# Kernel optimization log

Hardware: AMD Instinct MI355X
Metric: run time of the kernel (lower is better)

Reference implementation:

```python
import jax, jax.numpy as jnp
import numpy as np

N = 100000   # nodes
E = 1600000  # edges
NC = 10000   # candidates
G = 1000     # graphs
ND = 32      # node_emb_dim
ED = 8       # edge_emb_dim
L = 4        # num_layers


def setup_inputs() -> dict:
    key = jax.random.key(0)
    ks = jax.random.split(key, 12)
    s = 0.1
    return {
        "x": jax.random.normal(ks[0], (N, 2), dtype=jnp.float32),
        "edge_attr": jax.random.normal(ks[1], (E, 1), dtype=jnp.float32),
        "Wn_in": jax.random.normal(ks[2], (2, ND)) * s,
        "bn_in": jnp.zeros((ND,)),
        "We_in": jax.random.normal(ks[3], (1, ED)) * s,
        "be_in": jnp.zeros((ED,)),
        "We_l": jax.random.normal(ks[4], (L, 2 * ND + ED, ED)) * s,
        "be_l": jnp.zeros((L, ED)),
        "Wn_l": jax.random.normal(ks[5], (L, ND + ED, ND)) * s,
        "bn_l": jnp.zeros((L, ND)),
        "Wout": jax.random.normal(ks[6], (ND, 1)) * s,
        "bout": jnp.zeros((1,)),
        "edge_index": jax.random.randint(ks[7], (2, E), 0, N),
        "batch": jnp.sort(jax.random.randint(ks[8], (N,), 0, G)),
        "candidate_idxs": jax.random.randint(ks[9], (NC,), 0, N),
    }


def reference(x, edge_attr, Wn_in, bn_in, We_in, be_in, We_l, be_l, Wn_l, bn_l,
              Wout, bout, edge_index, batch, candidate_idxs):
    h = x @ Wn_in + bn_in            # [N, ND]
    e = edge_attr @ We_in + be_in    # [E, ED]
    src, dst = edge_index[0], edge_index[1]
    for l in range(L):
        # edge update: MLP on [x_src, x_dst, edge_attr]
        m = jnp.concatenate([h[src], h[dst], e], axis=-1)        # [E, 2*ND+ED]
        new_e = jax.nn.relu(m @ We_l[l] + be_l[l])               # [E, ED]
        # aggregate (aggr='add') messages at destination nodes
        agg = jax.ops.segment_sum(new_e, dst, num_segments=N)    # [N, ED]
        new_h = jax.nn.relu(jnp.concatenate([h, agg], axis=-1) @ Wn_l[l] + bn_l[l])
        h = h + new_h   # residual
        e = e + new_e   # residual
    logits = (h[candidate_idxs] @ Wout + bout)[:, 0]             # [NC]
    seg = batch[candidate_idxs]                                  # [NC] graph ids
    # scatter_log_softmax over per-graph candidate groups
    mx = jax.ops.segment_max(logits, seg, num_segments=G)
    shifted = logits - mx[seg]
    lse = jnp.log(jax.ops.segment_sum(jnp.exp(shifted), seg, num_segments=G))
    return shifted - lse[seg]
```

## Files before the change

kernel.cpp:

```cpp
#include <hip/hip_runtime.h>

#define ND 32
#define ED 8
#define NL 4
#define NG 1000
#define NBC_MAX 512
#define CHUNK 8192
#define CHUNK_H 4096

typedef unsigned short u16;

__device__ __forceinline__ int xcd_swizzle(int b, int nb) {
  int per = nb >> 3;
  return (b < (per << 3)) ? ((b & 7) * per + (b >> 3)) : b;
}


__device__ __forceinline__ unsigned pack2(float a, float b) {
  unsigned r;
  asm("v_cvt_pk_bf16_f32 %0, %1, %2" : "=v"(r) : "v"(a), "v"(b));
  return r;
}
__device__ __forceinline__ float bf_round(float f) {
  unsigned r;
  asm("v_cvt_pk_bf16_f32 %0, %1, %2" : "=v"(r) : "v"(f), "v"(f));
  return __uint_as_float(r << 16);
}
__device__ __forceinline__ void cvt8(uint4 p, float* o) {
  o[0] = __uint_as_float(p.x << 16); o[1] = __uint_as_float(p.x & 0xffff0000u);
  o[2] = __uint_as_float(p.y << 16); o[3] = __uint_as_float(p.y & 0xffff0000u);
  o[4] = __uint_as_float(p.z << 16); o[5] = __uint_as_float(p.z & 0xffff0000u);
  o[6] = __uint_as_float(p.w << 16); o[7] = __uint_as_float(p.w & 0xffff0000u);
}
__device__ __forceinline__ uint4 pack8(const float* v) {
  uint4 o;
  o.x = pack2(v[0], v[1]); o.y = pack2(v[2], v[3]);
  o.z = pack2(v[4], v[5]); o.w = pack2(v[6], v[7]);
  return o;
}


__global__ void k_chist(const int* __restrict__ dst, int* __restrict__ bcnt,
                        int E, int nbc) {
  __shared__ int lcnt[NBC_MAX];
  for (int b = threadIdx.x; b < nbc; b += blockDim.x) lcnt[b] = 0;
  __syncthreads();
  int e0 = blockIdx.x * CHUNK_H;
  int e1 = min(e0 + CHUNK_H, E);
  for (int i = e0 + threadIdx.x; i < e1; i += blockDim.x)
    atomicAdd(&lcnt[dst[i] >> 8], 1);
  __syncthreads();
  for (int b = threadIdx.x; b < nbc; b += blockDim.x)
    if (lcnt[b]) atomicAdd(&bcnt[b], lcnt[b]);
}

__global__ void k_cscan(const int* __restrict__ bcnt, int* __restrict__ bbase,
                        int nbc) {
  __shared__ int s[NBC_MAX];
  int tid = threadIdx.x;
  if (nbc <= NBC_MAX) {
    int v = (tid < nbc) ? bcnt[tid] : 0;
    s[tid] = v;
    __syncthreads();
    for (int st = 1; st < NBC_MAX; st <<= 1) {
      int t = (tid >= st) ? s[tid - st] : 0;
      __syncthreads();
      s[tid] += t;
      __syncthreads();
    }
    if (tid < nbc) bbase[tid] = s[tid] - v;
    if (tid == nbc - 1) bbase[nbc] = s[tid];
  } else if (tid == 0) {
    int run = 0;
    for (int i = 0; i < nbc; ++i) { bbase[i] = run; run += bcnt[i]; }
    bbase[nbc] = run;
  }
}

__global__ void k_binA(const int* __restrict__ src, const int* __restrict__ dst,
                       const float* __restrict__ ea,
                       const int* __restrict__ bbase, int* __restrict__ cursor_c,
                       uint2* __restrict__ binned, int E, int nbc) {
  __shared__ int lcnt[NBC_MAX];
  __shared__ int lbase[NBC_MAX];
  for (int b = threadIdx.x; b < nbc; b += blockDim.x) lcnt[b] = 0;
  __syncthreads();
  int e0 = blockIdx.x * CHUNK;
  int e1 = min(e0 + CHUNK, E);
  for (int i = e0 + threadIdx.x; i < e1; i += blockDim.x)
    atomicAdd(&lcnt[dst[i] >> 8], 1);
  __syncthreads();
  for (int b = threadIdx.x; b < nbc; b += blockDim.x) {
    int c = lcnt[b];
    lbase[b] = c ? (bbase[b] + atomicAdd(&cursor_c[b], c)) : 0;
  }
  __syncthreads();
  for (int i = e0 + threadIdx.x; i < e1; i += blockDim.x) {
    int d = dst[i];
    int pos = atomicAdd(&lbase[d >> 8], 1);
    binned[pos] = make_uint2((unsigned)src[i] | ((unsigned)(d & 255) << 24),
                             __float_as_uint(ea[i]));
  }
}

__global__ void k_binB_init(const uint2* __restrict__ binned,
                            const int* __restrict__ bbase,
                            int* __restrict__ ssrc, float* __restrict__ ea_s,
                            int* __restrict__ noffs,
                            const float* __restrict__ x,
                            const float* __restrict__ Wni,
                            const float* __restrict__ bni,
                            const float* __restrict__ We0,
                            const float* __restrict__ be0,
                            u16* __restrict__ h,
                            u16* __restrict__ zs, u16* __restrict__ zd,
                            int N) {
  __shared__ int hist[256];
  __shared__ int scn[256];
  int b = blockIdx.x;
  int base = bbase[b], end = bbase[b + 1];
  int node0 = b << 8;
  int nn = min(256, N - node0);
  hist[threadIdx.x] = 0;
  __syncthreads();
  for (int p = base + threadIdx.x; p < end; p += blockDim.x)
    atomicAdd(&hist[binned[p].x >> 24], 1);
  __syncthreads();
  int v = hist[threadIdx.x];
  scn[threadIdx.x] = v;
  __syncthreads();
  for (int st = 1; st < 256; st <<= 1) {
    int t = (threadIdx.x >= (unsigned)st) ? scn[threadIdx.x - st] : 0;
    __syncthreads();
    scn[threadIdx.x] += t;
    __syncthreads();
  }
  int excl = base + scn[threadIdx.x] - v;
  if ((int)threadIdx.x < nn) noffs[node0 + threadIdx.x] = excl;
  if (threadIdx.x == 0) noffs[min(node0 + 256, N)] = end;
  hist[threadIdx.x] = excl;
  __syncthreads();
  for (int p = base + threadIdx.x; p < end; p += blockDim.x) {
    uint2 rec = binned[p];
    int dl = (int)(rec.x >> 24);
    int pos = atomicAdd(&hist[dl], 1);
    ssrc[pos] = (int)(rec.x & 0xffffffu);
    ea_s[pos] = __uint_as_float(rec.y);
  }
  int n = node0 + threadIdx.x;
  if (n < N) {
    float x0 = x[2 * n], x1 = x[2 * n + 1];
    float vv[ND];
#pragma unroll
    for (int d = 0; d < ND; ++d)
      vv[d] = bf_round(fmaf(x0, Wni[d], fmaf(x1, Wni[ND + d], bni[d])));
    uint4* h4 = reinterpret_cast<uint4*>(h + (size_t)n * ND);
#pragma unroll
    for (int q = 0; q < 4; ++q) h4[q] = pack8(&vv[q * 8]);
    float zsv[ED], zdv[ED];
#pragma unroll
    for (int j = 0; j < ED; ++j) { zsv[j] = 0.0f; zdv[j] = be0[j]; }
#pragma unroll
    for (int k = 0; k < ND; ++k)
#pragma unroll
      for (int j = 0; j < ED; ++j) {
        zsv[j] = fmaf(vv[k], We0[k * ED + j], zsv[j]);
        zdv[j] = fmaf(vv[k], We0[(ND + k) * ED + j], zdv[j]);
      }
    *reinterpret_cast<uint4*>(zs + (size_t)n * ED) = pack8(zsv);
    *reinterpret_cast<uint4*>(zd + (size_t)n * ED) = pack8(zdv);
  }
}

template <int L0>
__global__ void k_layer(u16* __restrict__ h,
                        u16* __restrict__ e,
                        const float* __restrict__ ea_s,
                        const int* __restrict__ ssrc,
                        const int* __restrict__ noffs,
                        const u16* __restrict__ zs,
                        const u16* __restrict__ zd,
                        const float* __restrict__ Wei,
                        const float* __restrict__ bei,
                        const float* __restrict__ W3,
                        const float* __restrict__ Wn,
                        const float* __restrict__ bn,
                        const float* __restrict__ Wen,
                        const float* __restrict__ ben,
                        u16* __restrict__ zs_n, u16* __restrict__ zd_n,
                        int N) {
  int t = xcd_swizzle(blockIdx.x, gridDim.x) * blockDim.x + threadIdx.x;
  int n = t >> 3;
  int g = t & 7;
  if (n >= N) return;
  int o0 = noffs[n], o1 = noffs[n + 1];
  float zdv[ED];
  cvt8(*reinterpret_cast<const uint4*>(zd + (size_t)n * ED), zdv);
  const uint4* zs4 = reinterpret_cast<const uint4*>(zs);
  const uint4* e4c = reinterpret_cast<const uint4*>(e);
  uint4* e4 = reinterpret_cast<uint4*>(e);
  float av[ED];
#pragma unroll
  for (int j = 0; j < ED; ++j) av[j] = 0.0f;

  int p = o0 + g;
  int sA = 0, sB = 0;
  uint4 eA = make_uint4(0, 0, 0, 0), eB = make_uint4(0, 0, 0, 0);
  float aA = 0.0f, aB = 0.0f;
  uint4 zA = make_uint4(0, 0, 0, 0);
  if (p < o1) {
    sA = ssrc[p];
    if (L0) aA = ea_s[p]; else eA = e4c[p];
    zA = zs4[sA];
  }
  if (p + 8 < o1) {
    sB = ssrc[p + 8];
    if (L0) aB = ea_s[p + 8]; else eB = e4c[p + 8];
  }
  for (; p < o1; ) {
    int pn = p + 8, pc = p + 16;
    uint4 zB = make_uint4(0, 0, 0, 0);
    if (pn < o1) zB = zs4[sB];
    int sC = 0; uint4 eC = make_uint4(0, 0, 0, 0); float aC = 0.0f;
    if (pc < o1) {
      sC = ssrc[pc];
      if (L0) aC = ea_s[pc]; else eC = e4c[pc];
    }
    float zsv[ED], ein[ED], acc[ED];
    cvt8(zA, zsv);
    if (L0) {
#pragma unroll
      for (int j = 0; j < ED; ++j) ein[j] = fmaf(aA, Wei[j], bei[j]);
    } else {
      cvt8(eA, ein);
    }
#pragma unroll
    for (int j = 0; j < ED; ++j) acc[j] = zsv[j] + zdv[j];
#pragma unroll
    for (int k = 0; k < ED; ++k)
#pragma unroll
      for (int j = 0; j < ED; ++j)
        acc[j] = fmaf(ein[k], W3[k * ED + j], acc[j]);
    float eo[ED];
#pragma unroll
    for (int j = 0; j < ED; ++j) {
      float r = fmaxf(acc[j], 0.0f);
      av[j] += r;
      eo[j] = ein[j] + r;
    }
    e4[p] = pack8(eo);
    p = pn;
    sA = sB; eA = eB; aA = aB; zA = zB;
    sB = sC; eB = eC; aB = aC;
  }
#pragma unroll
  for (int j = 0; j < ED; ++j) {
    av[j] += __shfl_xor(av[j], 1);
    av[j] += __shfl_xor(av[j], 2);
    av[j] += __shfl_xor(av[j], 4);
  }
  uint4* h4 = reinterpret_cast<uint4*>(h + (size_t)n * ND);
  float hv[ND];
#pragma unroll
  for (int q = 0; q < 4; ++q) cvt8(h4[q], &hv[q * 8]);
  const int j0 = g * 4;
  float acc4[4];
#pragma unroll
  for (int jj = 0; jj < 4; ++jj) acc4[jj] = bn[j0 + jj];
#pragma unroll
  for (int k = 0; k < ND; ++k)
#pragma unroll
    for (int jj = 0; jj < 4; ++jj)
      acc4[jj] = fmaf(hv[k], Wn[k * ND + j0 + jj], acc4[jj]);
#pragma unroll
  for (int k = 0; k < ED; ++k)
#pragma unroll
    for (int jj = 0; jj < 4; ++jj)
      acc4[jj] = fmaf(av[k], Wn[(ND + k) * ND + j0 + jj], acc4[jj]);
  float hn4[4];
#pragma unroll
  for (int jj = 0; jj < 4; ++jj)
    hn4[jj] = bf_round(hv[j0 + jj] + fmaxf(acc4[jj], 0.0f));
  reinterpret_cast<uint2*>(h + (size_t)n * ND)[g] =
      make_uint2(pack2(hn4[0], hn4[1]), pack2(hn4[2], hn4[3]));
  float pz[2 * ED];
#pragma unroll
  for (int j = 0; j < 2 * ED; ++j) pz[j] = 0.0f;
#pragma unroll
  for (int kk = 0; kk < 4; ++kk) {
    float hk = hn4[kk];
    int krow = j0 + kk;
#pragma unroll
    for (int j = 0; j < ED; ++j) {
      pz[j] = fmaf(hk, Wen[krow * ED + j], pz[j]);
      pz[ED + j] = fmaf(hk, Wen[(ND + krow) * ED + j], pz[ED + j]);
    }
  }
#pragma unroll
  for (int j = 0; j < 2 * ED; ++j) {
    pz[j] += __shfl_xor(pz[j], 1);
    pz[j] += __shfl_xor(pz[j], 2);
    pz[j] += __shfl_xor(pz[j], 4);
  }
  if (g == 0) {
    *reinterpret_cast<uint4*>(zs_n + (size_t)n * ED) = pack8(pz);
  } else if (g == 1) {
    float zdo[ED];
#pragma unroll
    for (int j = 0; j < ED; ++j) zdo[j] = pz[ED + j] + ben[j];
    *reinterpret_cast<uint4*>(zd_n + (size_t)n * ED) = pack8(zdo);
  }
}


__device__ __forceinline__ unsigned int enc_f32(float f) {
  unsigned int bits = __float_as_uint(f);
  return (bits & 0x80000000u) ? ~bits : (bits | 0x80000000u);
}
__device__ __forceinline__ float dec_f32(unsigned int u) {
  unsigned int bits = (u & 0x80000000u) ? (u ^ 0x80000000u) : ~u;
  return __uint_as_float(bits);
}

__global__ void k_cand(const u16* __restrict__ h,
                       const u16* __restrict__ e,
                       const u16* __restrict__ zs,
                       const u16* __restrict__ zd,
                       const int* __restrict__ ssrc,
                       const int* __restrict__ noffs,
                       const int* __restrict__ cand,
                       const int* __restrict__ batch,
                       const float* __restrict__ W3,
                       const float* __restrict__ Wn,
                       const float* __restrict__ bn,
                       const float* __restrict__ Wout,
                       const float* __restrict__ bout,
                       float* __restrict__ logits,
                       int* __restrict__ seg,
                       unsigned int* __restrict__ mxu,
                       int NC) {
  int t = blockIdx.x * blockDim.x + threadIdx.x;
  int c = t >> 4, g = t & 15;
  if (c >= NC) return;
  int n = cand[c];
  int o0 = noffs[n], o1 = noffs[n + 1];
  const uint4* h4 = reinterpret_cast<const uint4*>(h + (size_t)n * ND);
  uint4 hq0 = h4[0], hq1 = h4[1], hq2 = h4[2], hq3 = h4[3];
  float zdv[ED];
  cvt8(*reinterpret_cast<const uint4*>(zd + (size_t)n * ED), zdv);
  const uint4* zs4 = reinterpret_cast<const uint4*>(zs);
  const uint4* e4c = reinterpret_cast<const uint4*>(e);
  float av[ED];
#pragma unroll
  for (int j = 0; j < ED; ++j) av[j] = 0.0f;

  auto cand_one = [&](uint4 z_, uint4 e_) {
    float zsv[ED], ein[ED], acc[ED];
    cvt8(z_, zsv);
    cvt8(e_, ein);
#pragma unroll
    for (int j = 0; j < ED; ++j) acc[j] = zsv[j] + zdv[j];
#pragma unroll
    for (int k = 0; k < ED; ++k)
#pragma unroll
      for (int j = 0; j < ED; ++j)
        acc[j] = fmaf(ein[k], W3[k * ED + j], acc[j]);
#pragma unroll
    for (int j = 0; j < ED; ++j) av[j] += fmaxf(acc[j], 0.0f);
  };

  for (int base = o0 + g; base < o1; base += 32) {
    bool v1 = base + 16 < o1;
    int pa = base;
    int pb = v1 ? base + 16 : base;
    int sa = ssrc[pa], sb = ssrc[pb];
    uint4 Ea = e4c[pa], Eb = e4c[pb];
    uint4 Za = zs4[sa], Zb = zs4[sb];
    cand_one(Za, Ea);
    if (v1) cand_one(Zb, Eb);
  }
#pragma unroll
  for (int j = 0; j < ED; ++j) {
    av[j] += __shfl_xor(av[j], 1);
    av[j] += __shfl_xor(av[j], 2);
    av[j] += __shfl_xor(av[j], 4);
    av[j] += __shfl_xor(av[j], 8);
  }
  float hv[ND];
  cvt8(hq0, &hv[0]); cvt8(hq1, &hv[8]); cvt8(hq2, &hv[16]); cvt8(hq3, &hv[24]);
  const int j0 = g * 2;
  float acc2[2];
#pragma unroll
  for (int jj = 0; jj < 2; ++jj) acc2[jj] = bn[j0 + jj];
#pragma unroll
  for (int k = 0; k < ND; ++k)
#pragma unroll
    for (int jj = 0; jj < 2; ++jj)
      acc2[jj] = fmaf(hv[k], Wn[k * ND + j0 + jj], acc2[jj]);
#pragma unroll
  for (int k = 0; k < ED; ++k)
#pragma unroll
    for (int jj = 0; jj < 2; ++jj)
      acc2[jj] = fmaf(av[k], Wn[(ND + k) * ND + j0 + jj], acc2[jj]);
  float lg = 0.0f;
#pragma unroll
  for (int jj = 0; jj < 2; ++jj)
    lg = fmaf(hv[j0 + jj] + fmaxf(acc2[jj], 0.0f), Wout[j0 + jj], lg);
  lg += __shfl_xor(lg, 1);
  lg += __shfl_xor(lg, 2);
  lg += __shfl_xor(lg, 4);
  lg += __shfl_xor(lg, 8);
  if (g == 0) {
    lg += bout[0];
    logits[c] = lg;
    int gr = batch[n];
    seg[c] = gr;
    atomicMax(&mxu[gr], enc_f32(lg));
  }
}

__global__ void k_expsum(float* __restrict__ logits,
                         const int* __restrict__ seg,
                         const unsigned int* __restrict__ mxu,
                         float* __restrict__ sum,
                         int NC) {
  int c = blockIdx.x * blockDim.x + threadIdx.x;
  if (c >= NC) return;
  int g = seg[c];
  float sh = logits[c] - dec_f32(mxu[g]);
  logits[c] = sh;
  atomicAdd(&sum[g], expf(sh));
}

__global__ void k_final(const float* __restrict__ shifted,
                        const int* __restrict__ seg,
                        const float* __restrict__ sum,
                        float* __restrict__ out, int NC) {
  int c = blockIdx.x * blockDim.x + threadIdx.x;
  if (c >= NC) return;
  out[c] = shifted[c] - logf(sum[seg[c]]);
}


extern "C" void kernel_launch(void* const* d_in, const int* in_sizes, int n_in,
                              void* d_out, int out_size, void* d_ws, size_t ws_size,
                              hipStream_t stream) {
  const float* x       = (const float*)d_in[0];
  const float* ea      = (const float*)d_in[1];
  const float* Wn_in   = (const float*)d_in[2];
  const float* bn_in   = (const float*)d_in[3];
  const float* We_in   = (const float*)d_in[4];
  const float* be_in   = (const float*)d_in[5];
  const float* We_l    = (const float*)d_in[6];
  const float* be_l    = (const float*)d_in[7];
  const float* Wn_l    = (const float*)d_in[8];
  const float* bn_l    = (const float*)d_in[9];
  const float* Wout    = (const float*)d_in[10];
  const float* bout    = (const float*)d_in[11];
  const int* edge_index= (const int*)d_in[12];
  const int* batch     = (const int*)d_in[13];
  const int* cand      = (const int*)d_in[14];

  const int N  = in_sizes[13];
  const int E  = in_sizes[1];
  const int NC = in_sizes[14];
  const int nbc = (N + 255) >> 8;

  char* ws = (char*)d_ws;
  uint2* binned = (uint2*)ws; ws += (size_t)E * sizeof(uint2);
  int*   ssrc   = (int*)ws;   ws += (size_t)E * sizeof(int);
  float* ea_s   = (float*)ws; ws += (size_t)E * sizeof(float);
  u16*   h      = (u16*)ws;   ws += (size_t)N * ND * sizeof(u16);
  u16*   e      = (u16*)ws;   ws += (size_t)E * ED * sizeof(u16);
  u16*   zs0    = (u16*)ws;   ws += (size_t)N * ED * sizeof(u16);
  u16*   zd0    = (u16*)ws;   ws += (size_t)N * ED * sizeof(u16);
  u16*   zs1    = (u16*)ws;   ws += (size_t)N * ED * sizeof(u16);
  u16*   zd1    = (u16*)ws;   ws += (size_t)N * ED * sizeof(u16);
  int*   noffs  = (int*)ws;   ws += ((size_t)N + 4) * sizeof(int);
  int*   bcnt   = (int*)ws;   ws += (size_t)NBC_MAX * sizeof(int);
  int*   cursor = (int*)ws;   ws += (size_t)NBC_MAX * sizeof(int);
  unsigned int* mxu = (unsigned int*)ws; ws += (size_t)NG * sizeof(unsigned int);
  float* sum    = (float*)ws; ws += (size_t)NG * sizeof(float);
  int*   bbase  = (int*)ws;   ws += ((size_t)NBC_MAX + 4) * sizeof(int);
  float* logits = (float*)ws; ws += (size_t)NC * sizeof(float);
  int*   seg    = (int*)ws;   ws += (size_t)NC * sizeof(int);

  const int* srcp = edge_index;
  const int* dstp = edge_index + E;
  const int blk = 256;
  const size_t WE_STRIDE = (size_t)(2 * ND + ED) * ED;

  hipMemsetAsync(bcnt, 0, (2 * (size_t)NBC_MAX + 2 * (size_t)NG) * sizeof(int),
                 stream);

  k_chist<<<(E + CHUNK_H - 1) / CHUNK_H, 1024, 0, stream>>>(dstp, bcnt, E, nbc);
  k_cscan<<<1, NBC_MAX, 0, stream>>>(bcnt, bbase, nbc);
  k_binA<<<(E + CHUNK - 1) / CHUNK, 1024, 0, stream>>>(srcp, dstp, ea, bbase,
                                                       cursor, binned, E, nbc);
  k_binB_init<<<nbc, 256, 0, stream>>>(binned, bbase, ssrc, ea_s, noffs,
                                       x, Wn_in, bn_in, We_l, be_l,
                                       h, zs0, zd0, N);

  const int ngrid8 = (N + 31) / 32;
  u16* zsc = zs0; u16* zdc = zd0;
  u16* zsn = zs1; u16* zdn = zd1;
  for (int l = 0; l < NL - 1; ++l) {
    const float* W3 = We_l + l * WE_STRIDE + (size_t)2 * ND * ED;
    const float* Wn = Wn_l + (size_t)l * (ND + ED) * ND;
    const float* bn = bn_l + (size_t)l * ND;
    const float* Wen = We_l + (l + 1) * WE_STRIDE;
    const float* ben = be_l + (size_t)(l + 1) * ED;
    if (l == 0) {
      k_layer<1><<<ngrid8, 256, 0, stream>>>(
          h, e, ea_s, ssrc, noffs, zsc, zdc, We_in, be_in, W3, Wn, bn,
          Wen, ben, zsn, zdn, N);
    } else {
      k_layer<0><<<ngrid8, 256, 0, stream>>>(
          h, e, ea_s, ssrc, noffs, zsc, zdc, We_in, be_in, W3, Wn, bn,
          Wen, ben, zsn, zdn, N);
    }
    u16* t;
    t = zsc; zsc = zsn; zsn = t;
    t = zdc; zdc = zdn; zdn = t;
  }

  {
    const int l = NL - 1;
    const float* W3 = We_l + l * WE_STRIDE + (size_t)2 * ND * ED;
    const float* Wn = Wn_l + (size_t)l * (ND + ED) * ND;
    const float* bn = bn_l + (size_t)l * ND;
    k_cand<<<((size_t)NC * 16 + 255) / 256, 256, 0, stream>>>(
        h, e, zsc, zdc, ssrc, noffs, cand, batch, W3, Wn, bn, Wout, bout,
        logits, seg, mxu, NC);
  }
  k_expsum<<<(NC + blk - 1) / blk, blk, 0, stream>>>(logits, seg, mxu, sum, NC);
  k_final<<<(NC + blk - 1) / blk, blk, 0, stream>>>(logits, seg, sum,
                                                    (float*)d_out, NC);
}
```

Measured before the change: 331.8 us.

## Replace two-level bucket sort with direct per-node counting sort using global atomics

Builds the destination-sorted CSR by counting edges per node with global atomics, scanning node counts in one block, and scattering edges via per-node atomic cursors, fused with node embedding init. This removes the intermediate binned buffer and the two-pass coarse/fine bucketing. In exchange it relies on heavy global atomic traffic, a serial-heavy single-block scan, and edge order within a node becomes nondeterministic.

```diff
diff --git a/kernel.cpp b/kernel.cpp
--- a/kernel.cpp
+++ b/kernel.cpp
@@ -4,9 +4,6 @@
 #define ED 8
 #define NL 4
 #define NG 1000
-#define NBC_MAX 512
-#define CHUNK 8192
-#define CHUNK_H 4096
 
 typedef unsigned short u16;
 
@@ -40,121 +37,68 @@
 }
 
 
-__global__ void k_chist(const int* __restrict__ dst, int* __restrict__ bcnt,
-                        int E, int nbc) {
-  __shared__ int lcnt[NBC_MAX];
-  for (int b = threadIdx.x; b < nbc; b += blockDim.x) lcnt[b] = 0;
+__global__ void k_nhist(const int* __restrict__ dst, int* __restrict__ ncnt,
+                        int E) {
+  int i = blockIdx.x * blockDim.x + threadIdx.x;
+  if (i < E) atomicAdd(&ncnt[dst[i]], 1);
+}
+
+__global__ void k_nscan(const int* __restrict__ ncnt, int* __restrict__ noffs,
+                        int* __restrict__ cur, int N, int E) {
+  __shared__ int s[1024];
+  int t = threadIdx.x;
+  int C = (N + 1023) >> 10;
+  int lo = t * C, hi = min(lo + C, N);
+  int run = 0;
+  for (int i = lo; i < hi; ++i) {
+    int v = ncnt[i];
+    noffs[i] = run;
+    run += v;
+  }
+  s[t] = run;
   __syncthreads();
-  int e0 = blockIdx.x * CHUNK_H;
-  int e1 = min(e0 + CHUNK_H, E);
-  for (int i = e0 + threadIdx.x; i < e1; i += blockDim.x)
-    atomicAdd(&lcnt[dst[i] >> 8], 1);
-  __syncthreads();
-  for (int b = threadIdx.x; b < nbc; b += blockDim.x)
-    if (lcnt[b]) atomicAdd(&bcnt[b], lcnt[b]);
-}
-
-__global__ void k_cscan(const int* __restrict__ bcnt, int* __restrict__ bbase,
-                        int nbc) {
-  __shared__ int s[NBC_MAX];
-  int tid = threadIdx.x;
-  if (nbc <= NBC_MAX) {
-    int v = (tid < nbc) ? bcnt[tid] : 0;
-    s[tid] = v;
+  for (int st = 1; st < 1024; st <<= 1) {
+    int v = (t >= st) ? s[t - st] : 0;
     __syncthreads();
-    for (int st = 1; st < NBC_MAX; st <<= 1) {
-      int t = (tid >= st) ? s[tid - st] : 0;
-      __syncthreads();
-      s[tid] += t;
-      __syncthreads();
-    }
-    if (tid < nbc) bbase[tid] = s[tid] - v;
-    if (tid == nbc - 1) bbase[nbc] = s[tid];
-  } else if (tid == 0) {
-    int run = 0;
-    for (int i = 0; i < nbc; ++i) { bbase[i] = run; run += bcnt[i]; }
-    bbase[nbc] = run;
-  }
-}
-
-__global__ void k_binA(const int* __restrict__ src, const int* __restrict__ dst,
-                       const float* __restrict__ ea,
-                       const int* __restrict__ bbase, int* __restrict__ cursor_c,
-                       uint2* __restrict__ binned, int E, int nbc) {
-  __shared__ int lcnt[NBC_MAX];
-  __shared__ int lbase[NBC_MAX];
-  for (int b = threadIdx.x; b < nbc; b += blockDim.x) lcnt[b] = 0;
-  __syncthreads();
-  int e0 = blockIdx.x * CHUNK;
-  int e1 = min(e0 + CHUNK, E);
-  for (int i = e0 + threadIdx.x; i < e1; i += blockDim.x)
-    atomicAdd(&lcnt[dst[i] >> 8], 1);
-  __syncthreads();
-  for (int b = threadIdx.x; b < nbc; b += blockDim.x) {
-    int c = lcnt[b];
-    lbase[b] = c ? (bbase[b] + atomicAdd(&cursor_c[b], c)) : 0;
-  }
-  __syncthreads();
-  for (int i = e0 + threadIdx.x; i < e1; i += blockDim.x) {
+    s[t] += v;
+    __syncthreads();
+  }
+  int base = s[t] - run;
+  for (int i = lo; i < hi; ++i) {
+    int v = noffs[i] + base;
+    noffs[i] = v;
+    cur[i] = v;
+  }
+  if (t == 0) noffs[N] = E;
+}
+
+__global__ void k_scatter_init(const int* __restrict__ src,
+                               const int* __restrict__ dst,
+                               const float* __restrict__ ea,
+                               int* __restrict__ cur,
+                               int* __restrict__ ssrc, float* __restrict__ ea_s,
+                               const float* __restrict__ x,
+                               const float* __restrict__ Wni,
+                               const float* __restrict__ bni,
+                               const float* __restrict__ We0,
+                               const float* __restrict__ be0,
+                               u16* __restrict__ h,
+                               u16* __restrict__ zs, u16* __restrict__ zd,
+                               int E, int N) {
+  int i = blockIdx.x * blockDim.x + threadIdx.x;
+  if (i < E) {
     int d = dst[i];
-    int pos = atomicAdd(&lbase[d >> 8], 1);
-    binned[pos] = make_uint2((unsigned)src[i] | ((unsigned)(d & 255) << 24),
-                             __float_as_uint(ea[i]));
-  }
-}
-
-__global__ void k_binB_init(const uint2* __restrict__ binned,
-                            const int* __restrict__ bbase,
-                            int* __restrict__ ssrc, float* __restrict__ ea_s,
-                            int* __restrict__ noffs,
-                            const float* __restrict__ x,
-                            const float* __restrict__ Wni,
-                            const float* __restrict__ bni,
-                            const float* __restrict__ We0,
-                            const float* __restrict__ be0,
-                            u16* __restrict__ h,
-                            u16* __restrict__ zs, u16* __restrict__ zd,
-                            int N) {
-  __shared__ int hist[256];
-  __shared__ int scn[256];
-  int b = blockIdx.x;
-  int base = bbase[b], end = bbase[b + 1];
-  int node0 = b << 8;
-  int nn = min(256, N - node0);
-  hist[threadIdx.x] = 0;
-  __syncthreads();
-  for (int p = base + threadIdx.x; p < end; p += blockDim.x)
-    atomicAdd(&hist[binned[p].x >> 24], 1);
-  __syncthreads();
-  int v = hist[threadIdx.x];
-  scn[threadIdx.x] = v;
-  __syncthreads();
-  for (int st = 1; st < 256; st <<= 1) {
-    int t = (threadIdx.x >= (unsigned)st) ? scn[threadIdx.x - st] : 0;
-    __syncthreads();
-    scn[threadIdx.x] += t;
-    __syncthreads();
-  }
-  int excl = base + scn[threadIdx.x] - v;
-  if ((int)threadIdx.x < nn) noffs[node0 + threadIdx.x] = excl;
-  if (threadIdx.x == 0) noffs[min(node0 + 256, N)] = end;
-  hist[threadIdx.x] = excl;
-  __syncthreads();
-  for (int p = base + threadIdx.x; p < end; p += blockDim.x) {
-    uint2 rec = binned[p];
-    int dl = (int)(rec.x >> 24);
-    int pos = atomicAdd(&hist[dl], 1);
-    ssrc[pos] = (int)(rec.x & 0xffffffu);
-    ea_s[pos] = __uint_as_float(rec.y);
-  }
-  int n = node0 + threadIdx.x;
-  if (n < N) {
-    float x0 = x[2 * n], x1 = x[2 * n + 1];
+    int pos = atomicAdd(&cur[d], 1);
+    ssrc[pos] = src[i];
+    ea_s[pos] = ea[i];
+  }
+  if (i < N) {
+    float x0 = x[2 * i], x1 = x[2 * i + 1];
     float vv[ND];
 #pragma unroll
     for (int d = 0; d < ND; ++d)
       vv[d] = bf_round(fmaf(x0, Wni[d], fmaf(x1, Wni[ND + d], bni[d])));
-    uint4* h4 = reinterpret_cast<uint4*>(h + (size_t)n * ND);
+    uint4* h4 = reinterpret_cast<uint4*>(h + (size_t)i * ND);
 #pragma unroll
     for (int q = 0; q < 4; ++q) h4[q] = pack8(&vv[q * 8]);
     float zsv[ED], zdv[ED];
@@ -167,8 +111,8 @@
         zsv[j] = fmaf(vv[k], We0[k * ED + j], zsv[j]);
         zdv[j] = fmaf(vv[k], We0[(ND + k) * ED + j], zdv[j]);
       }
-    *reinterpret_cast<uint4*>(zs + (size_t)n * ED) = pack8(zsv);
-    *reinterpret_cast<uint4*>(zd + (size_t)n * ED) = pack8(zdv);
+    *reinterpret_cast<uint4*>(zs + (size_t)i * ED) = pack8(zsv);
+    *reinterpret_cast<uint4*>(zd + (size_t)i * ED) = pack8(zdv);
   }
 }
 
@@ -464,10 +408,8 @@
   const int N  = in_sizes[13];
   const int E  = in_sizes[1];
   const int NC = in_sizes[14];
-  const int nbc = (N + 255) >> 8;
 
   char* ws = (char*)d_ws;
-  uint2* binned = (uint2*)ws; ws += (size_t)E * sizeof(uint2);
   int*   ssrc   = (int*)ws;   ws += (size_t)E * sizeof(int);
   float* ea_s   = (float*)ws; ws += (size_t)E * sizeof(float);
   u16*   h      = (u16*)ws;   ws += (size_t)N * ND * sizeof(u16);
@@ -477,11 +419,10 @@
   u16*   zs1    = (u16*)ws;   ws += (size_t)N * ED * sizeof(u16);
   u16*   zd1    = (u16*)ws;   ws += (size_t)N * ED * sizeof(u16);
   int*   noffs  = (int*)ws;   ws += ((size_t)N + 4) * sizeof(int);
-  int*   bcnt   = (int*)ws;   ws += (size_t)NBC_MAX * sizeof(int);
-  int*   cursor = (int*)ws;   ws += (size_t)NBC_MAX * sizeof(int);
+  int*   cur    = (int*)ws;   ws += ((size_t)N + 4) * sizeof(int);
+  int*   ncnt   = (int*)ws;   ws += (size_t)N * sizeof(int);
   unsigned int* mxu = (unsigned int*)ws; ws += (size_t)NG * sizeof(unsigned int);
   float* sum    = (float*)ws; ws += (size_t)NG * sizeof(float);
-  int*   bbase  = (int*)ws;   ws += ((size_t)NBC_MAX + 4) * sizeof(int);
   float* logits = (float*)ws; ws += (size_t)NC * sizeof(float);
   int*   seg    = (int*)ws;   ws += (size_t)NC * sizeof(int);
 
@@ -490,16 +431,13 @@
   const int blk = 256;
   const size_t WE_STRIDE = (size_t)(2 * ND + ED) * ED;
 
-  hipMemsetAsync(bcnt, 0, (2 * (size_t)NBC_MAX + 2 * (size_t)NG) * sizeof(int),
-                 stream);
-
-  k_chist<<<(E + CHUNK_H - 1) / CHUNK_H, 1024, 0, stream>>>(dstp, bcnt, E, nbc);
-  k_cscan<<<1, NBC_MAX, 0, stream>>>(bcnt, bbase, nbc);
-  k_binA<<<(E + CHUNK - 1) / CHUNK, 1024, 0, stream>>>(srcp, dstp, ea, bbase,
-                                                       cursor, binned, E, nbc);
-  k_binB_init<<<nbc, 256, 0, stream>>>(binned, bbase, ssrc, ea_s, noffs,
-                                       x, Wn_in, bn_in, We_l, be_l,
-                                       h, zs0, zd0, N);
+  hipMemsetAsync(ncnt, 0, ((size_t)N + 2 * (size_t)NG) * sizeof(int), stream);
+
+  k_nhist<<<(E + blk - 1) / blk, blk, 0, stream>>>(dstp, ncnt, E);
+  k_nscan<<<1, 1024, 0, stream>>>(ncnt, noffs, cur, N, E);
+  k_scatter_init<<<(E + blk - 1) / blk, blk, 0, stream>>>(
+      srcp, dstp, ea, cur, ssrc, ea_s, x, Wn_in, bn_in, We_l, be_l,
+      h, zs0, zd0, E, N);
 
   const int ngrid8 = (N + 31) / 32;
   u16* zsc = zs0; u16* zdc = zd0;
```

After: 734.8 us. 121% more time.

## Fuse layer, candidate and softmax kernels into one cooperative persistent kernel

Applied to the files above, without the earlier changes.

Replaces the per-layer k_layer launches plus k_cand, k_expsum and k_final with a single cooperative kernel that loops over layers using grid-stride loops and grid.sync() between stages. The goal is to remove several kernel launch gaps and tail effects between short dependent stages. In exchange the grid is capped at occupancy-limited resident blocks. The mega kernel uses the union of both bodies' registers, which may lower occupancy and slow the memory-bound layer phases. A fallback to the old multi-kernel path is kept if the cooperative launch fails.

```diff
diff --git a/kernel.cpp b/kernel.cpp
--- a/kernel.cpp
+++ b/kernel.cpp
@@ -1,4 +1,7 @@
 #include <hip/hip_runtime.h>
+#include <hip/hip_cooperative_groups.h>
+
+namespace cg = cooperative_groups;
 
 #define ND 32
 #define ED 8
@@ -7,6 +10,7 @@
 #define NBC_MAX 512
 #define CHUNK 8192
 #define CHUNK_H 4096
+#define WE_STRIDE ((size_t)(2 * ND + ED) * ED)
 
 typedef unsigned short u16;
 
@@ -37,6 +41,15 @@
   o.x = pack2(v[0], v[1]); o.y = pack2(v[2], v[3]);
   o.z = pack2(v[4], v[5]); o.w = pack2(v[6], v[7]);
   return o;
+}
+
+__device__ __forceinline__ unsigned int enc_f32(float f) {
+  unsigned int bits = __float_as_uint(f);
+  return (bits & 0x80000000u) ? ~bits : (bits | 0x80000000u);
+}
+__device__ __forceinline__ float dec_f32(unsigned int u) {
+  unsigned int bits = (u & 0x80000000u) ? (u ^ 0x80000000u) : ~u;
+  return __uint_as_float(bits);
 }
 
 
@@ -173,26 +186,15 @@
 }
 
 template <int L0>
-__global__ void k_layer(u16* __restrict__ h,
-                        u16* __restrict__ e,
-                        const float* __restrict__ ea_s,
-                        const int* __restrict__ ssrc,
-                        const int* __restrict__ noffs,
-                        const u16* __restrict__ zs,
-                        const u16* __restrict__ zd,
-                        const float* __restrict__ Wei,
-                        const float* __restrict__ bei,
-                        const float* __restrict__ W3,
-                        const float* __restrict__ Wn,
-                        const float* __restrict__ bn,
-                        const float* __restrict__ Wen,
-                        const float* __restrict__ ben,
-                        u16* __restrict__ zs_n, u16* __restrict__ zd_n,
-                        int N) {
-  int t = xcd_swizzle(blockIdx.x, gridDim.x) * blockDim.x + threadIdx.x;
-  int n = t >> 3;
-  int g = t & 7;
-  if (n >= N) return;
+__device__ __forceinline__ void layer_body(
+    int n, int g, u16* __restrict__ h, u16* __restrict__ e,
+    const float* __restrict__ ea_s, const int* __restrict__ ssrc,
+    const int* __restrict__ noffs, const u16* __restrict__ zs,
+    const u16* __restrict__ zd, const float* __restrict__ Wei,
+    const float* __restrict__ bei, const float* __restrict__ W3,
+    const float* __restrict__ Wn, const float* __restrict__ bn,
+    const float* __restrict__ Wen, const float* __restrict__ ben,
+    u16* __restrict__ zs_n, u16* __restrict__ zd_n) {
   int o0 = noffs[n], o1 = noffs[n + 1];
   float zdv[ED];
   cvt8(*reinterpret_cast<const uint4*>(zd + (size_t)n * ED), zdv);
@@ -312,36 +314,15 @@
   }
 }
 
-
-__device__ __forceinline__ unsigned int enc_f32(float f) {
-  unsigned int bits = __float_as_uint(f);
-  return (bits & 0x80000000u) ? ~bits : (bits | 0x80000000u);
-}
-__device__ __forceinline__ float dec_f32(unsigned int u) {
-  unsigned int bits = (u & 0x80000000u) ? (u ^ 0x80000000u) : ~u;
-  return __uint_as_float(bits);
-}
-
-__global__ void k_cand(const u16* __restrict__ h,
-                       const u16* __restrict__ e,
-                       const u16* __restrict__ zs,
-                       const u16* __restrict__ zd,
-                       const int* __restrict__ ssrc,
-                       const int* __restrict__ noffs,
-                       const int* __restrict__ cand,
-                       const int* __restrict__ batch,
-                       const float* __restrict__ W3,
-                       const float* __restrict__ Wn,
-                       const float* __restrict__ bn,
-                       const float* __restrict__ Wout,
-                       const float* __restrict__ bout,
-                       float* __restrict__ logits,
-                       int* __restrict__ seg,
-                       unsigned int* __restrict__ mxu,
-                       int NC) {
-  int t = blockIdx.x * blockDim.x + threadIdx.x;
-  int c = t >> 4, g = t & 15;
-  if (c >= NC) return;
+__device__ __forceinline__ void cand_body(
+    int c, int g, const u16* __restrict__ h, const u16* __restrict__ e,
+    const u16* __restrict__ zs, const u16* __restrict__ zd,
+    const int* __restrict__ ssrc, const int* __restrict__ noffs,
+    const int* __restrict__ cand, const int* __restrict__ batch,
+    const float* __restrict__ W3, const float* __restrict__ Wn,
+    const float* __restrict__ bn, const float* __restrict__ Wout,
+    const float* __restrict__ bout, float* __restrict__ logits,
+    int* __restrict__ seg, unsigned int* __restrict__ mxu) {
   int n = cand[c];
   int o0 = noffs[n], o1 = noffs[n + 1];
   const uint4* h4 = reinterpret_cast<const uint4*>(h + (size_t)n * ND);
@@ -419,11 +400,53 @@
   }
 }
 
+
+template <int L0>
+__global__ void k_layer(u16* __restrict__ h, u16* __restrict__ e,
+                        const float* __restrict__ ea_s,
+                        const int* __restrict__ ssrc,
+                        const int* __restrict__ noffs,
+                        const u16* __restrict__ zs, const u16* __restrict__ zd,
+                        const float* __restrict__ Wei,
+                        const float* __restrict__ bei,
+                        const float* __restrict__ W3,
+                        const float* __restrict__ Wn,
+                        const float* __restrict__ bn,
+                        const float* __restrict__ Wen,
+                        const float* __restrict__ ben,
+                        u16* __restrict__ zs_n, u16* __restrict__ zd_n,
+                        int N) {
+  int t = xcd_swizzle(blockIdx.x, gridDim.x) * blockDim.x + threadIdx.x;
+  int n = t >> 3, g = t & 7;
+  if (n >= N) return;
+  layer_body<L0>(n, g, h, e, ea_s, ssrc, noffs, zs, zd, Wei, bei, W3, Wn, bn,
+                 Wen, ben, zs_n, zd_n);
+}
+
+__global__ void k_cand(const u16* __restrict__ h, const u16* __restrict__ e,
+                       const u16* __restrict__ zs, const u16* __restrict__ zd,
+                       const int* __restrict__ ssrc,
+                       const int* __restrict__ noffs,
+                       const int* __restrict__ cand,
+                       const int* __restrict__ batch,
+                       const float* __restrict__ W3,
+                       const float* __restrict__ Wn,
+                       const float* __restrict__ bn,
+                       const float* __restrict__ Wout,
+                       const float* __restrict__ bout,
+                       float* __restrict__ logits, int* __restrict__ seg,
+                       unsigned int* __restrict__ mxu, int NC) {
+  int t = blockIdx.x * blockDim.x + threadIdx.x;
+  int c = t >> 4, g = t & 15;
+  if (c >= NC) return;
+  cand_body(c, g, h, e, zs, zd, ssrc, noffs, cand, batch, W3, Wn, bn, Wout,
+            bout, logits, seg, mxu);
+}
+
 __global__ void k_expsum(float* __restrict__ logits,
                          const int* __restrict__ seg,
                          const unsigned int* __restrict__ mxu,
-                         float* __restrict__ sum,
-                         int NC) {
+                         float* __restrict__ sum, int NC) {
   int c = blockIdx.x * blockDim.x + threadIdx.x;
   if (c >= NC) return;
   int g = seg[c];
@@ -439,6 +462,74 @@
   int c = blockIdx.x * blockDim.x + threadIdx.x;
   if (c >= NC) return;
   out[c] = shifted[c] - logf(sum[seg[c]]);
+}
+
+
+struct MegaArgs {
+  u16 *h, *e;
+  const float* ea_s;
+  const int* ssrc;
+  const int* noffs;
+  u16 *zs0, *zd0, *zs1, *zd1;
+  const float *We_in, *be_in, *We_l, *be_l, *Wn_l, *bn_l;
+  const int *cand, *batch;
+  const float *Wout, *bout;
+  float* logits;
+  int* seg;
+  unsigned int* mxu;
+  float* sum;
+  float* out;
+  int N, NC;
+};
+
+__global__ void k_mega(MegaArgs a) {
+  cg::grid_group grid = cg::this_grid();
+  const long gid = (long)blockIdx.x * blockDim.x + threadIdx.x;
+  const long GT = (long)gridDim.x * blockDim.x;
+  u16 *zsc = a.zs0, *zdc = a.zd0, *zsn = a.zs1, *zdn = a.zd1;
+  for (int l = 0; l < NL - 1; ++l) {
+    const float* W3 = a.We_l + l * WE_STRIDE + (size_t)2 * ND * ED;
+    const float* Wn = a.Wn_l + (size_t)l * (ND + ED) * ND;
+    const float* bn = a.bn_l + (size_t)l * ND;
+    const float* Wen = a.We_l + (l + 1) * WE_STRIDE;
+    const float* ben = a.be_l + (size_t)(l + 1) * ED;
+    const long TT = (long)a.N * 8;
+    for (long t = gid; t < TT; t += GT) {
+      int n = (int)(t >> 3), g = (int)(t & 7);
+      if (l == 0)
+        layer_body<1>(n, g, a.h, a.e, a.ea_s, a.ssrc, a.noffs, zsc, zdc,
+                      a.We_in, a.be_in, W3, Wn, bn, Wen, ben, zsn, zdn);
+      else
+        layer_body<0>(n, g, a.h, a.e, a.ea_s, a.ssrc, a.noffs, zsc, zdc,
+                      a.We_in, a.be_in, W3, Wn, bn, Wen, ben, zsn, zdn);
+    }
+    grid.sync();
+    u16* tp;
+    tp = zsc; zsc = zsn; zsn = tp;
+    tp = zdc; zdc = zdn; zdn = tp;
+  }
+  {
+    const int l = NL - 1;
+    const float* W3 = a.We_l + l * WE_STRIDE + (size_t)2 * ND * ED;
+    const float* Wn = a.Wn_l + (size_t)l * (ND + ED) * ND;
+    const float* bn = a.bn_l + (size_t)l * ND;
+    const long TT = (long)a.NC * 16;
+    for (long t = gid; t < TT; t += GT) {
+      int c = (int)(t >> 4), g = (int)(t & 15);
+      cand_body(c, g, a.h, a.e, zsc, zdc, a.ssrc, a.noffs, a.cand, a.batch,
+                W3, Wn, bn, a.Wout, a.bout, a.logits, a.seg, a.mxu);
+    }
+  }
+  grid.sync();
+  for (long c = gid; c < a.NC; c += GT) {
+    int g = a.seg[c];
+    float sh = a.logits[c] - dec_f32(a.mxu[g]);
+    a.logits[c] = sh;
+    atomicAdd(&a.sum[g], expf(sh));
+  }
+  grid.sync();
+  for (long c = gid; c < a.NC; c += GT)
+    a.out[c] = a.logits[c] - logf(a.sum[a.seg[c]]);
 }
 
 
@@ -488,7 +579,6 @@
   const int* srcp = edge_index;
   const int* dstp = edge_index + E;
   const int blk = 256;
-  const size_t WE_STRIDE = (size_t)(2 * ND + ED) * ED;
 
   hipMemsetAsync(bcnt, 0, (2 * (size_t)NBC_MAX + 2 * (size_t)NG) * sizeof(int),
                  stream);
@@ -501,39 +591,70 @@
                                        x, Wn_in, bn_in, We_l, be_l,
                                        h, zs0, zd0, N);
 
-  const int ngrid8 = (N + 31) / 32;
-  u16* zsc = zs0; u16* zdc = zd0;
-  u16* zsn = zs1; u16* zdn = zd1;
-  for (int l = 0; l < NL - 1; ++l) {
-    const float* W3 = We_l + l * WE_STRIDE + (size_t)2 * ND * ED;
-    const float* Wn = Wn_l + (size_t)l * (ND + ED) * ND;
-    const float* bn = bn_l + (size_t)l * ND;
-    const float* Wen = We_l + (l + 1) * WE_STRIDE;
-    const float* ben = be_l + (size_t)(l + 1) * ED;
-    if (l == 0) {
-      k_layer<1><<<ngrid8, 256, 0, stream>>>(
-          h, e, ea_s, ssrc, noffs, zsc, zdc, We_in, be_in, W3, Wn, bn,
-          Wen, ben, zsn, zdn, N);
-    } else {
-      k_layer<0><<<ngrid8, 256, 0, stream>>>(
-          h, e, ea_s, ssrc, noffs, zsc, zdc, We_in, be_in, W3, Wn, bn,
-          Wen, ben, zsn, zdn, N);
-    }
-    u16* t;
-    t = zsc; zsc = zsn; zsn = t;
-    t = zdc; zdc = zdn; zdn = t;
-  }
-
-  {
-    const int l = NL - 1;
-    const float* W3 = We_l + l * WE_STRIDE + (size_t)2 * ND * ED;
-    const float* Wn = Wn_l + (size_t)l * (ND + ED) * ND;
-    const float* bn = bn_l + (size_t)l * ND;
-    k_cand<<<((size_t)NC * 16 + 255) / 256, 256, 0, stream>>>(
-        h, e, zsc, zdc, ssrc, noffs, cand, batch, W3, Wn, bn, Wout, bout,
-        logits, seg, mxu, NC);
-  }
-  k_expsum<<<(NC + blk - 1) / blk, blk, 0, stream>>>(logits, seg, mxu, sum, NC);
-  k_final<<<(NC + blk - 1) / blk, blk, 0, stream>>>(logits, seg, sum,
-                                                    (float*)d_out, NC);
-}
+  static int coop_blocks = -2;
+  if (coop_blocks == -2) {
+    int per_cu = 0;
+    hipError_t oe =
+        hipOccupancyMaxActiveBlocksPerMultiprocessor(&per_cu, k_mega, 256, 0);
+    int ncu = 0;
+    hipDeviceProp_t prop;
+    int dev = 0;
+    if (oe == hipSuccess && hipGetDevice(&dev) == hipSuccess &&
+        hipGetDeviceProperties(&prop, dev) == hipSuccess)
+      ncu = prop.multiProcessorCount;
+    coop_blocks = (per_cu > 0 && ncu > 0) ? per_cu * ncu : -1;
+  }
+
+  bool done = false;
+  if (coop_blocks > 0) {
+    long need = ((long)N * 8 + 255) / 256;
+    int grid = (int)((need < coop_blocks) ? need : coop_blocks);
+    if (grid < 1) grid = 1;
+    MegaArgs args = {h, e, ea_s, ssrc, noffs, zs0, zd0, zs1, zd1,
+                     We_in, be_in, We_l, be_l, Wn_l, bn_l, cand, batch,
+                     Wout, bout, logits, seg, mxu, sum, (float*)d_out, N, NC};
+    void* kargs[] = {&args};
+    hipError_t le = hipLaunchCooperativeKernel(
+        (const void*)k_mega, dim3(grid), dim3(256), kargs, 0, stream);
+    if (le == hipSuccess) done = true;
+    else coop_blocks = -1;
+  }
+
+  if (!done) {
+    const int ngrid8 = (N + 31) / 32;
+    u16* zsc = zs0; u16* zdc = zd0;
+    u16* zsn = zs1; u16* zdn = zd1;
+    for (int l = 0; l < NL - 1; ++l) {
+      const float* W3 = We_l + l * WE_STRIDE + (size_t)2 * ND * ED;
+      const float* Wn = Wn_l + (size_t)l * (ND + ED) * ND;
+      const float* bn = bn_l + (size_t)l * ND;
+      const float* Wen = We_l + (l + 1) * WE_STRIDE;
+      const float* ben = be_l + (size_t)(l + 1) * ED;
+      if (l == 0) {
+        k_layer<1><<<ngrid8, 256, 0, stream>>>(
+            h, e, ea_s, ssrc, noffs, zsc, zdc, We_in, be_in, W3, Wn, bn,
+            Wen, ben, zsn, zdn, N);
+      } else {
+        k_layer<0><<<ngrid8, 256, 0, stream>>>(
+            h, e, ea_s, ssrc, noffs, zsc, zdc, We_in, be_in, W3, Wn, bn,
+            Wen, ben, zsn, zdn, N);
+      }
+      u16* t;
+      t = zsc; zsc = zsn; zsn = t;
+      t = zdc; zdc = zdn; zdn = t;
+    }
+    {
+      const int l = NL - 1;
+      const float* W3 = We_l + l * WE_STRIDE + (size_t)2 * ND * ED;
+      const float* Wn = Wn_l + (size_t)l * (ND + ED) * ND;
+      const float* bn = bn_l + (size_t)l * ND;
+      k_cand<<<((size_t)NC * 16 + 255) / 256, 256, 0, stream>>>(
+          h, e, zsc, zdc, ssrc, noffs, cand, batch, W3, Wn, bn, Wout, bout,
+          logits, seg, mxu, NC);
+    }
+    k_expsum<<<(NC + blk - 1) / blk, blk, 0, stream>>>(logits, seg, mxu, sum,
+                                                       NC);
+    k_final<<<(NC + blk - 1) / blk, blk, 0, stream>>>(logits, seg, sum,
+                                                      (float*)d_out, NC);
+  }
+}
```

New measurement: 804.5 us. +142.4%, slower.
